# Performance work log

Hardware: AMD Instinct MI355X
Metric: run time of the kernel (lower is better)

## Reference

```python
import jax, jax.numpy as jnp
import numpy as np

DIM = 1024
HEADS = 16
DIM_HEAD = 64
INNER = HEADS * DIM_HEAD
B, M, N = 8, 4096, 256
EPS = 1e-5


def layer_norm(x, g, b):
    mu = jnp.mean(x, axis=-1, keepdims=True)
    var = jnp.mean(jnp.square(x - mu), axis=-1, keepdims=True)
    return (x - mu) * jax.lax.rsqrt(var + EPS) * g + b


def setup_inputs() -> dict:
    key = jax.random.key(0)
    ks = jax.random.split(key, 8)
    x = jax.random.normal(ks[0], (B, M, DIM), dtype=jnp.float32)
    latents = jax.random.normal(ks[1], (B, N, DIM), dtype=jnp.float32)
    x_att_mask = jax.random.randint(ks[2], (B, M), 0, 2) == 1  # True = masked
    s = 0.02
    Wq = jax.random.normal(ks[3], (DIM, INNER), dtype=jnp.float32) * s
    Wkv = jax.random.normal(ks[4], (DIM, 2 * INNER), dtype=jnp.float32) * s
    Wo = jax.random.normal(ks[5], (INNER, DIM), dtype=jnp.float32) * s
    return {
        "x": x, "latents": latents, "x_att_mask": x_att_mask,
        "nm_g": jnp.ones((DIM,), jnp.float32), "nm_b": jnp.zeros((DIM,), jnp.float32),
        "nl_g": jnp.ones((DIM,), jnp.float32), "nl_b": jnp.zeros((DIM,), jnp.float32),
        "Wq": Wq, "Wkv": Wkv, "Wo": Wo,
    }


def reference(x, latents, x_att_mask, nm_g, nm_b, nl_g, nl_b, Wq, Wkv, Wo):
    b, n, d = latents.shape
    h, dh = HEADS, DIM_HEAD
    scale = dh ** (-0.5)

    # additive mask: concat(media mask, all-False latent mask); True -> -inf, False -> +1 (faithful quirk)
    latent_mask = jnp.zeros((b, n), dtype=bool)
    full_mask = jnp.concatenate([x_att_mask, latent_mask], axis=1)  # [b, m+n]
    add_mask = jnp.where(full_mask, -jnp.inf, 1.0).astype(x.dtype)[:, None, None, :]  # [b,1,1,m+n]

    xn = layer_norm(x, nm_g, nm_b)
    ln = layer_norm(latents, nl_g, nl_b)

    q = (ln @ Wq).reshape(b, n, h, dh).transpose(0, 2, 1, 3)  # bhnd
    kv_in = jnp.concatenate([xn, ln], axis=1)                 # [b, m+n, d]
    kv = kv_in @ Wkv
    k, v = jnp.split(kv, 2, axis=-1)
    j = kv_in.shape[1]
    k = k.reshape(b, j, h, dh).transpose(0, 2, 1, 3)
    v = v.reshape(b, j, h, dh).transpose(0, 2, 1, 3)

    sim = jnp.einsum('bhid,bhjd->bhij', q * scale, k)
    sim = sim - jnp.max(sim, axis=-1, keepdims=True)
    sim = sim + add_mask
    attn = jax.nn.softmax(sim, axis=-1)
    out = jnp.einsum('bhij,bhjd->bhid', attn, v)
    out = out.transpose(0, 2, 1, 3).reshape(b, n, h * dh)
    return out @ Wo
```

## Files before the change

### kernel.cpp

```cpp
#include <hip/hip_runtime.h>
#include <hip/hip_bf16.h>
#include <stdint.h>

#define HEADS 16
#define DH    64
#define NB    8
#define MQ    256
#define MX    4096
#define JD    4352
#define DIMV  1024
#define GK    1024

typedef __bf16 bf16;
typedef __bf16 bf16x8 __attribute__((ext_vector_type(8)));
typedef float  f32x4  __attribute__((ext_vector_type(4)));

#define SWZ(r, c) (((c) ^ ((r) & 7)))

#define VMW(n) asm volatile("s_waitcnt vmcnt(" #n ")" ::: "memory")

__device__ __forceinline__ void gl_lds16(const void* g, void* l) {
  __builtin_amdgcn_global_load_lds((const __attribute__((address_space(1))) void*)g,
                                   (__attribute__((address_space(3))) void*)l, 16, 0, 0);
}

__global__ __launch_bounds__(256) void ln_kernel(
    const float* __restrict__ X, const float* __restrict__ gw, const float* __restrict__ bw,
    bf16* __restrict__ out_kv, bf16* __restrict__ out_ln, int is_lat)
{
  const int row = blockIdx.x;
  const int tid = threadIdx.x;
  const float4 v = ((const float4*)(X + (size_t)row * DIMV))[tid];
  float s  = v.x + v.y + v.z + v.w;
  float s2 = v.x*v.x + v.y*v.y + v.z*v.z + v.w*v.w;
#pragma unroll
  for (int m = 1; m < 64; m <<= 1) { s += __shfl_xor(s, m); s2 += __shfl_xor(s2, m); }
  __shared__ float red[8];
  const int wid = tid >> 6;
  if ((tid & 63) == 0) { red[wid*2] = s; red[wid*2+1] = s2; }
  __syncthreads();
  s  = red[0] + red[2] + red[4] + red[6];
  s2 = red[1] + red[3] + red[5] + red[7];
  const float mu  = s * (1.0f / DIMV);
  const float var = s2 * (1.0f / DIMV) - mu * mu;
  const float rst = rsqrtf(var + 1e-5f);
  const float4 g4 = ((const float4*)gw)[tid];
  const float4 b4 = ((const float4*)bw)[tid];
  union { bf16 h[4]; short4 s4; } u;
  u.h[0] = (bf16)((v.x - mu) * rst * g4.x + b4.x);
  u.h[1] = (bf16)((v.y - mu) * rst * g4.y + b4.y);
  u.h[2] = (bf16)((v.z - mu) * rst * g4.z + b4.z);
  u.h[3] = (bf16)((v.w - mu) * rst * g4.w + b4.w);
  size_t kvrow;
  if (is_lat) { int b = row >> 8;  int i = row & 255;  kvrow = (size_t)b * JD + MX + i; }
  else        { int b = row >> 12; int j = row & 4095; kvrow = (size_t)b * JD + j; }
  *(short4*)(out_kv + kvrow * DIMV + tid * 4) = u.s4;
  if (is_lat) *(short4*)(out_ln + (size_t)row * DIMV + tid * 4) = u.s4;
}

__global__ __launch_bounds__(256) void transpose_w(
    const float* __restrict__ in, bf16* __restrict__ out, int R, int C)
{
  __shared__ float t[64][65];
  const int tilesC = C >> 6;
  const int tc = blockIdx.x % tilesC, tr = blockIdx.x / tilesC;
  const int r0 = tr << 6, c0 = tc << 6;
  const int lr = threadIdx.x >> 4;
  const int lc = (threadIdx.x & 15) << 2;
#pragma unroll
  for (int p = 0; p < 4; p++) {
    float4 v = *(const float4*)&in[(size_t)(r0 + lr + p*16) * C + c0 + lc];
    t[lr + p*16][lc    ] = v.x; t[lr + p*16][lc + 1] = v.y;
    t[lr + p*16][lc + 2] = v.z; t[lr + p*16][lc + 3] = v.w;
  }
  __syncthreads();
#pragma unroll
  for (int p = 0; p < 4; p++) {
    const int oc = lr + p*16;
    union { bf16 h[4]; short4 s4; } u;
    u.h[0] = (bf16)t[lc    ][oc]; u.h[1] = (bf16)t[lc + 1][oc];
    u.h[2] = (bf16)t[lc + 2][oc]; u.h[3] = (bf16)t[lc + 3][oc];
    *(short4*)&out[(size_t)(c0 + oc) * R + r0 + lc] = u.s4;
  }
}

__global__ __launch_bounds__(256) void mask_detect(
    const unsigned char* __restrict__ m, int n, int* __restrict__ flag)
{
  const int tid = threadIdx.x;
  int cnt = 0;
  for (int i = tid; i < n; i += 256) cnt += (m[i] != 0) ? 1 : 0;
#pragma unroll
  for (int mm = 1; mm < 64; mm <<= 1) cnt += __shfl_xor(cnt, mm);
  __shared__ int r4[4];
  if ((tid & 63) == 0) r4[tid >> 6] = cnt;
  __syncthreads();
  if (tid == 0) {
    int t = r4[0] + r4[1] + r4[2] + r4[3];
    flag[0] = (t * 16 > n * 5) ? 1 : 0;
  }
}

__global__ __launch_bounds__(256) void mask_build(
    const void* __restrict__ mraw, const int* __restrict__ flag, float* __restrict__ mm)
{
  const int idx = blockIdx.x * 256 + threadIdx.x;
  const int b = idx / JD, j = idx - b * JD;
  float v = 1.0f;
  if (j < MX) {
    bool masked = (*flag) ? (((const unsigned char*)mraw)[b * MX + j] != 0)
                          : (((const int*)mraw)[b * MX + j] != 0);
    v = masked ? 0.0f : 1.0f;
  }
  mm[idx] = v;
}

__global__ __launch_bounds__(512, 2) void gemm256(
    const bf16* __restrict__ A, const bf16* __restrict__ Bt,
    const bf16* __restrict__ Aq, const bf16* __restrict__ Bq,
    bf16* __restrict__ outR, bf16* __restrict__ outVT, bf16* __restrict__ outQ)
{
  __shared__ bf16 sm[65536];

  const int tid = threadIdx.x;
  const int lane = tid & 63, wid = tid >> 6;
  const int wr = wid >> 2, wc = wid & 3;
  const int lc = lane & 15, lq = lane >> 4;
  const int srow = tid >> 3, sc = tid & 7;
  const int ssw = SWZ(srow, sc) * 8;

  int bid = blockIdx.x;
  bid = (bid & 7) * 140 + (bid >> 3);

  const bf16 *Arow, *Brow;
  int m0, n0, omode;
  if (bid < 1088) {
    const int by = bid >> 3, bx = bid & 7;
    m0 = by * 256;
    if (bx < 4) { n0 = bx * 256;
      Arow = A  + (size_t)m0 * GK; Brow = Bt + (size_t)n0 * GK; omode = 0; }
    else        { n0 = 1024 + (bx - 4) * 256;
      Arow = Bt + (size_t)n0 * GK; Brow = A  + (size_t)m0 * GK; omode = 1; }
  } else {
    const int ix = bid - 1088;
    m0 = (ix >> 2) * 256; n0 = (ix & 3) * 256;
    Arow = Aq + (size_t)m0 * GK; Brow = Bq + (size_t)n0 * GK; omode = 2;
  }

  const bf16* Abase = Arow + (size_t)srow * GK + ssw;
  const bf16* Bbase = Brow + (size_t)srow * GK + ssw;

  auto stA = [&](int d, int h, int kt) {
#pragma unroll
    for (int l = 0; l < 2; ++l)
      gl_lds16(Abase + (size_t)(h*128 + l*64) * GK + kt * 64,
               &sm[d*32768 + (h*128 + l*64)*64 + tid*8]);
  };
  auto stB = [&](int d, int h, int kt) {
#pragma unroll
    for (int l = 0; l < 2; ++l)
      gl_lds16(Bbase + (size_t)(h*128 + l*64) * GK + kt * 64,
               &sm[d*32768 + 16384 + (h*128 + l*64)*64 + tid*8]);
  };

  f32x4 acc[8][4];
#pragma unroll
  for (int i = 0; i < 8; i++)
#pragma unroll
    for (int j = 0; j < 4; j++)
#pragma unroll
      for (int r = 0; r < 4; r++) acc[i][j][r] = 0.f;

#define DS_PHASE(d, q, STAGE_STMT, WAIT_STMT)                                  \
  {                                                                            \
    const bf16* As_ = sm + (d)*32768;                                          \
    const bf16* Bs_ = sm + (d)*32768 + 16384;                                  \
    bf16x8 af[2][2];                                                           \
    _Pragma("unroll") for (int mi = 0; mi < 2; ++mi)                           \
      _Pragma("unroll") for (int kk = 0; kk < 2; ++kk)                         \
        af[mi][kk] = *(const bf16x8*)&As_[(wr*128 + ((q)*2+mi)*16 + lc)*64 +   \
                                          SWZ(lc, kk*4 + lq)*8];               \
    if ((q) == 0) {                                                            \
      _Pragma("unroll") for (int n = 0; n < 4; ++n)                            \
        _Pragma("unroll") for (int kk = 0; kk < 2; ++kk)                       \
          bfrag[n][kk] = *(const bf16x8*)&Bs_[(wc*64 + n*16 + lc)*64 +         \
                                              SWZ(lc, kk*4 + lq)*8];           \
    }                                                                          \
    STAGE_STMT;                                                                \
    WAIT_STMT;                                                                 \
    __builtin_amdgcn_s_barrier();                                              \
    __builtin_amdgcn_s_setprio(1);                                             \
    _Pragma("unroll") for (int kk = 0; kk < 2; ++kk)                           \
      _Pragma("unroll") for (int mi = 0; mi < 2; ++mi)                         \
        _Pragma("unroll") for (int n = 0; n < 4; ++n)                          \
          acc[(q)*2+mi][n] = __builtin_amdgcn_mfma_f32_16x16x32_bf16(          \
              af[mi][kk], bfrag[n][kk], acc[(q)*2+mi][n], 0, 0, 0);            \
    __builtin_amdgcn_s_setprio(0);                                             \
    __builtin_amdgcn_s_barrier();                                              \
  }

  stB(0, 0, 0); stB(0, 1, 0);
  stA(0, 0, 0); stA(0, 1, 0);
  stB(1, 0, 1); stB(1, 1, 1);
  VMW(4);
  __builtin_amdgcn_s_barrier();

  bf16x8 bfrag[4][2];
#pragma unroll 1
  for (int it = 0; it < 8; ++it) {
    const int tb = 2*it + 1, ta2 = 2*it + 2, tb2 = 2*it + 3;
    const bool s2 = (ta2 < 16), s3 = (tb2 < 16);
    DS_PHASE(0, 0, { stA(1, 0, tb); stA(1, 1, tb); }, {});
    DS_PHASE(0, 1, { if (s2) stB(0, 0, ta2); }, {});
    DS_PHASE(0, 2, { if (s2) stB(0, 1, ta2); }, {});
    DS_PHASE(0, 3, {}, { if (s2) { VMW(4); } else { VMW(0); } });
    DS_PHASE(1, 0, { if (s2) stA(0, 0, ta2); }, {});
    DS_PHASE(1, 1, { if (s2) stA(0, 1, ta2); }, {});
    DS_PHASE(1, 2, { if (s3) stB(1, 0, tb2); }, {});
    DS_PHASE(1, 3, { if (s3) stB(1, 1, tb2); }, { if (s3) { VMW(4); } });
  }
#undef DS_PHASE

  __syncthreads();
  bf16* Ct = sm;
#pragma unroll
  for (int m = 0; m < 8; ++m)
#pragma unroll
    for (int n = 0; n < 4; ++n) {
      const int col = wc*64 + n*16 + lc;
      const int cch = col >> 3, cw = col & 7;
#pragma unroll
      for (int r = 0; r < 4; ++r) {
        const int row = wr*128 + m*16 + lq*4 + r;
        Ct[row*256 + (((cch ^ (row & 31)) << 3) + cw)] = (bf16)acc[m][n][r];
      }
    }
  __syncthreads();

  const int cch = tid & 31, r0 = tid >> 5;
  if (omode != 1) {
    bf16* dst0 = (omode == 0 ? outR : outQ);
#pragma unroll
    for (int i = 0; i < 16; ++i) {
      const int row = r0 + i*16;
      bf16x8 v = *(const bf16x8*)&Ct[row*256 + ((cch ^ (row & 31)) << 3)];
      *(bf16x8*)(dst0 + (size_t)(m0 + row) * 1024 + n0 + cch*8) = v;
    }
  } else {
    const int bb = m0 / JD;
    const int jbase = m0 - bb * JD;
#pragma unroll
    for (int i = 0; i < 16; ++i) {
      const int row = r0 + i*16;
      const int cc = n0 + row - 1024;
      bf16x8 v = *(const bf16x8*)&Ct[row*256 + ((cch ^ (row & 31)) << 3)];
      bf16* dst = outVT + (((size_t)(bb*HEADS + (cc >> 6)))*64 + (cc & 63)) * JD
                        + jbase + cch*8;
      *(bf16x8*)dst = v;
    }
  }
}

__global__ __launch_bounds__(256) void gemm128(
    const bf16* __restrict__ A, const bf16* __restrict__ Bt,
    float* __restrict__ Cf, int N)
{
  __shared__ bf16 smem[2 * 128 * 64];
  bf16* As = smem;
  bf16* Bs = smem + 128 * 64;

  const int tid = threadIdx.x;
  const int lane = tid & 63, wid = tid >> 6;
  const int wr = wid >> 1, wc = wid & 1;
  const int m0 = blockIdx.y * 128;
  const int n0 = blockIdx.x * 128;
  const int srow = tid >> 3, sc = tid & 7;
  const int ssw = SWZ(srow, sc) * 8;
  const int lc = lane & 15, lq = lane >> 4;

  f32x4 acc[4][4];
#pragma unroll
  for (int i = 0; i < 4; i++)
#pragma unroll
    for (int j = 0; j < 4; j++)
#pragma unroll
      for (int r = 0; r < 4; r++) acc[i][j][r] = 0.f;

  const bf16* Abase = A + (size_t)m0 * GK + (size_t)srow * GK + ssw;
  const bf16* Bbase = Bt + (size_t)n0 * GK + (size_t)srow * GK + ssw;

  for (int k0 = 0; k0 < GK; k0 += 64) {
    __syncthreads();
#pragma unroll
    for (int q = 0; q < 4; q++) {
      gl_lds16(Abase + (size_t)q * 32 * GK + k0, &As[(srow + q*32) * 64 + sc*8]);
      gl_lds16(Bbase + (size_t)q * 32 * GK + k0, &Bs[(srow + q*32) * 64 + sc*8]);
    }
    VMW(0);
    __syncthreads();
#pragma unroll
    for (int kk = 0; kk < 2; kk++) {
      bf16x8 af[4], bfr[4];
#pragma unroll
      for (int mi = 0; mi < 4; mi++)
        af[mi] = *(const bf16x8*)&As[(wr*64 + mi*16 + lc) * 64 + SWZ(lc, kk*4 + lq)*8];
#pragma unroll
      for (int ni = 0; ni < 4; ni++)
        bfr[ni] = *(const bf16x8*)&Bs[(wc*64 + ni*16 + lc) * 64 + SWZ(lc, kk*4 + lq)*8];
#pragma unroll
      for (int mi = 0; mi < 4; mi++)
#pragma unroll
        for (int ni = 0; ni < 4; ni++)
          acc[mi][ni] = __builtin_amdgcn_mfma_f32_16x16x32_bf16(af[mi], bfr[ni], acc[mi][ni], 0, 0, 0);
    }
  }

#pragma unroll
  for (int mi = 0; mi < 4; mi++)
#pragma unroll
    for (int ni = 0; ni < 4; ni++) {
      const int r = m0 + wr*64 + mi*16 + lq*4;
      const int c = n0 + wc*64 + ni*16 + lc;
#pragma unroll
      for (int reg = 0; reg < 4; reg++)
        Cf[(size_t)(r + reg) * N + c] = acc[mi][ni][reg];
    }
}

__global__ __launch_bounds__(512) void attn_kernel(
    const bf16* __restrict__ Qrows,
    const bf16* __restrict__ Krows,
    const bf16* __restrict__ VT,
    const float* __restrict__ mmul,
    bf16* __restrict__ outp)
{
  const int bh = blockIdx.x >> 1, qt = blockIdx.x & 1;
  const int b = bh >> 4, h = bh & 15;
  __shared__ bf16 Qs[128 * 64];
  __shared__ bf16 Ks[2][64 * 64];
  __shared__ bf16 VTs[2][64 * 64];
  __shared__ bf16 Ps[8][16 * 64];
  const int tid = threadIdx.x, lane = tid & 63, w = tid >> 6;
  const int lc = lane & 15, lq = lane >> 4;
  const int srow = tid >> 3, sc = tid & 7;
  const int ssw = SWZ(srow, sc) * 8;

  const bf16* Qg = Qrows + ((size_t)(b*MQ + qt*128)) * 1024 + h*64;
  const bf16* Kg = Krows + ((size_t)b * JD) * 1024 + h*64;
  const bf16* Vg = VT + ((size_t)bh * 64) * JD;

  auto stKV = [&](int c, int t) {
    gl_lds16(Kg + (size_t)(t*64 + srow) * 1024 + ssw, &Ks[c][tid*8]);
    gl_lds16(Vg + (size_t)srow * JD + t*64 + ssw, &VTs[c][tid*8]);
  };

  gl_lds16(Qg + (size_t)srow * 1024 + ssw, &Qs[tid*8]);
  gl_lds16(Qg + (size_t)(srow + 64) * 1024 + ssw, &Qs[(tid + 512)*8]);
  stKV(0, 0);
  stKV(1, 1);
  VMW(2);
  __syncthreads();

  bf16x8 qf[2];
#pragma unroll
  for (int kk = 0; kk < 2; kk++)
    qf[kk] = *(const bf16x8*)&Qs[(w*16 + lc) * 64 + SWZ(lc, kk*4 + lq)*8];

  char* PsW = (char*)&Ps[w][0];
  f32x4 oacc[4];
  float den = 0.f;
#pragma unroll
  for (int di = 0; di < 4; di++)
#pragma unroll
    for (int r = 0; r < 4; r++) oacc[di][r] = 0.f;

#pragma unroll 1
  for (int t = 0; t < JD/64; ++t) {
    const int c = t & 1;
    const int j0 = t * 64;

    f32x4 sacc[4];
#pragma unroll
    for (int nj = 0; nj < 4; nj++)
#pragma unroll
      for (int r = 0; r < 4; r++) sacc[nj][r] = 0.f;
#pragma unroll
    for (int kk = 0; kk < 2; kk++) {
      bf16x8 kf[4];
#pragma unroll
      for (int nj = 0; nj < 4; nj++)
        kf[nj] = *(const bf16x8*)&Ks[c][(nj*16 + lc) * 64 + SWZ(lc, kk*4 + lq)*8];
#pragma unroll
      for (int nj = 0; nj < 4; nj++)
        sacc[nj] = __builtin_amdgcn_mfma_f32_16x16x32_bf16(kf[nj], qf[kk], sacc[nj], 0, 0, 0);
    }

#pragma unroll
    for (int nj = 0; nj < 4; nj++) {
      const float4 mm4 = *(const float4*)&mmul[b * JD + j0 + nj*16 + lq*4];
      const float p0 = exp2f(sacc[nj][0] * 0.18033688f) * mm4.x;
      const float p1 = exp2f(sacc[nj][1] * 0.18033688f) * mm4.y;
      const float p2 = exp2f(sacc[nj][2] * 0.18033688f) * mm4.z;
      const float p3 = exp2f(sacc[nj][3] * 0.18033688f) * mm4.w;
      den += (p0 + p1) + (p2 + p3);
      union { bf16 h[4]; uint2 u2; } pu;
      pu.h[0] = (bf16)p0; pu.h[1] = (bf16)p1; pu.h[2] = (bf16)p2; pu.h[3] = (bf16)p3;
      const int c4s = (nj*2 + (lq >> 1)) ^ (lc & 7);
      *(uint2*)(PsW + lc*128 + (c4s << 4) + ((lq & 1) << 3)) = pu.u2;
    }

#pragma unroll
    for (int kk = 0; kk < 2; kk++) {
      bf16x8 pf = *(const bf16x8*)(PsW + lc*128 + ((((kk << 2) + lq) ^ (lc & 7)) << 4));
#pragma unroll
      for (int di = 0; di < 4; di++) {
        bf16x8 vf = *(const bf16x8*)&VTs[c][(di*16 + lc) * 64 + SWZ(lc, kk*4 + lq)*8];
        oacc[di] = __builtin_amdgcn_mfma_f32_16x16x32_bf16(pf, vf, oacc[di], 0, 0, 0);
      }
    }

    __builtin_amdgcn_s_barrier();
    if (t + 2 < JD/64) {
      stKV(c, t + 2);
      VMW(2);
    } else if (t + 1 < JD/64) {
      VMW(0);
    }
    __builtin_amdgcn_s_barrier();
  }

  den += __shfl_xor(den, 16);
  den += __shfl_xor(den, 32);
  const float rden = 1.0f / den;

#pragma unroll
  for (int di = 0; di < 4; di++) {
    const int col = h*64 + di*16 + lc;
#pragma unroll
    for (int r = 0; r < 4; r++) {
      const float dr = __shfl(rden, lq*4 + r, 16);
      const int i = qt*128 + w*16 + lq*4 + r;
      outp[(size_t)(b*MQ + i) * 1024 + col] = (bf16)(oacc[di][r] * dr);
    }
  }
}

extern "C" void kernel_launch(void* const* d_in, const int* in_sizes, int n_in,
                              void* d_out, int out_size, void* d_ws, size_t ws_size,
                              hipStream_t stream)
{
  const float* x    = (const float*)d_in[0];
  const float* lat  = (const float*)d_in[1];
  const void*  mraw = d_in[2];
  const float* nm_g = (const float*)d_in[3];
  const float* nm_b = (const float*)d_in[4];
  const float* nl_g = (const float*)d_in[5];
  const float* nl_b = (const float*)d_in[6];
  const float* Wq   = (const float*)d_in[7];
  const float* Wkv  = (const float*)d_in[8];
  const float* Wo   = (const float*)d_in[9];
  float* out = (float*)d_out;

  char* p = (char*)d_ws;
  auto alloc = [&](size_t bytes) { char* r = p; p += (bytes + 255) & ~(size_t)255; return r; };

  bf16*  kv_in  = (bf16*)alloc((size_t)NB * JD * DIMV * 2);
  bf16*  Krows  = (bf16*)alloc((size_t)NB * JD * 1024 * 2);
  bf16*  VTbuf  = (bf16*)alloc((size_t)NB * HEADS * 64 * JD * 2);
  bf16*  WqT    = (bf16*)alloc((size_t)1024 * 1024 * 2);
  bf16*  WkvT   = (bf16*)alloc((size_t)2048 * 1024 * 2);
  bf16*  WoT    = (bf16*)alloc((size_t)1024 * 1024 * 2);
  bf16*  ln_buf = (bf16*)alloc((size_t)NB * MQ * DIMV * 2);
  bf16*  Qrows  = (bf16*)alloc((size_t)NB * MQ * 1024 * 2);
  bf16*  attout = (bf16*)alloc((size_t)NB * MQ * DIMV * 2);
  float* mmulp  = (float*)alloc((size_t)NB * JD * 4);
  int*   flag   = (int*)alloc(256);
  (void)ws_size; (void)in_sizes; (void)n_in; (void)out_size;

  ln_kernel<<<NB * MX, 256, 0, stream>>>(x,   nm_g, nm_b, kv_in, nullptr, 0);
  ln_kernel<<<NB * MQ, 256, 0, stream>>>(lat, nl_g, nl_b, kv_in, ln_buf, 1);
  transpose_w<<<256, 256, 0, stream>>>(Wq,  WqT,  1024, 1024);
  transpose_w<<<512, 256, 0, stream>>>(Wkv, WkvT, 1024, 2048);
  transpose_w<<<256, 256, 0, stream>>>(Wo,  WoT,  1024, 1024);
  mask_detect<<<1, 256, 0, stream>>>((const unsigned char*)mraw, 32768, flag);
  mask_build<<<136, 256, 0, stream>>>(mraw, flag, mmulp);

  gemm256<<<1120, 512, 0, stream>>>(kv_in, WkvT, ln_buf, WqT, Krows, VTbuf, Qrows);
  attn_kernel<<<256, 512, 0, stream>>>(Qrows, Krows, VTbuf, mmulp, attout);
  gemm128<<<dim3(8, 16), 256, 0, stream>>>(attout, WoT, out, 1024);
}
```

Measured before the change: 524.5 us.

## Deepen attention K/V prefetch to four stages and stage additive mask in LDS

The attention kernel's K/V ring buffer grows from two to four stages, so loads are issued further ahead of their use. The whole per-batch mask row is preloaded into shared memory once. The mask becomes additive (a large negative bias folded into the exp2 argument with an fma), replacing a global float4 load and a multiply every tile. This raises LDS use per block to roughly 100KB, which may cut occupancy, and the additive bias only approximates zeroing masked terms.

```diff
diff --git a/kernel.cpp b/kernel.cpp
--- a/kernel.cpp
+++ b/kernel.cpp
@@ -102,17 +102,17 @@
 }
 
 __global__ __launch_bounds__(256) void mask_build(
-    const void* __restrict__ mraw, const int* __restrict__ flag, float* __restrict__ mm)
+    const void* __restrict__ mraw, const int* __restrict__ flag, float* __restrict__ madd)
 {
   const int idx = blockIdx.x * 256 + threadIdx.x;
   const int b = idx / JD, j = idx - b * JD;
-  float v = 1.0f;
+  float v = 0.0f;
   if (j < MX) {
     bool masked = (*flag) ? (((const unsigned char*)mraw)[b * MX + j] != 0)
                           : (((const int*)mraw)[b * MX + j] != 0);
-    v = masked ? 0.0f : 1.0f;
-  }
-  mm[idx] = v;
+    v = masked ? -20000.0f : 0.0f;
+  }
+  madd[idx] = v;
 }
 
 __global__ __launch_bounds__(512, 2) void gemm256(
@@ -331,15 +331,16 @@
     const bf16* __restrict__ Qrows,
     const bf16* __restrict__ Krows,
     const bf16* __restrict__ VT,
-    const float* __restrict__ mmul,
+    const float* __restrict__ madd,
     bf16* __restrict__ outp)
 {
   const int bh = blockIdx.x >> 1, qt = blockIdx.x & 1;
   const int b = bh >> 4, h = bh & 15;
   __shared__ bf16 Qs[128 * 64];
-  __shared__ bf16 Ks[2][64 * 64];
-  __shared__ bf16 VTs[2][64 * 64];
+  __shared__ bf16 Ks[4][64 * 64];
+  __shared__ bf16 VTs[4][64 * 64];
   __shared__ bf16 Ps[8][16 * 64];
+  __shared__ float Madd[JD];
   const int tid = threadIdx.x, lane = tid & 63, w = tid >> 6;
   const int lc = lane & 15, lq = lane >> 4;
   const int srow = tid >> 3, sc = tid & 7;
@@ -348,6 +349,7 @@
   const bf16* Qg = Qrows + ((size_t)(b*MQ + qt*128)) * 1024 + h*64;
   const bf16* Kg = Krows + ((size_t)b * JD) * 1024 + h*64;
   const bf16* Vg = VT + ((size_t)bh * 64) * JD;
+  const float* mp = madd + (size_t)b * JD;
 
   auto stKV = [&](int c, int t) {
     gl_lds16(Kg + (size_t)(t*64 + srow) * 1024 + ssw, &Ks[c][tid*8]);
@@ -356,9 +358,12 @@
 
   gl_lds16(Qg + (size_t)srow * 1024 + ssw, &Qs[tid*8]);
   gl_lds16(Qg + (size_t)(srow + 64) * 1024 + ssw, &Qs[(tid + 512)*8]);
-  stKV(0, 0);
-  stKV(1, 1);
-  VMW(2);
+  gl_lds16(mp + tid*4,        &Madd[tid*4]);
+  gl_lds16(mp + 2048 + tid*4, &Madd[2048 + tid*4]);
+  if (tid < 64) gl_lds16(mp + 4096 + tid*4, &Madd[4096 + tid*4]);
+  VMW(0);
+  stKV(0, 0); stKV(1, 1); stKV(2, 2); stKV(3, 3);
+  VMW(6);
   __syncthreads();
 
   bf16x8 qf[2];
@@ -376,7 +381,7 @@
 
 #pragma unroll 1
   for (int t = 0; t < JD/64; ++t) {
-    const int c = t & 1;
+    const int c = t & 3;
     const int j0 = t * 64;
 
     f32x4 sacc[4];
@@ -397,11 +402,11 @@
 
 #pragma unroll
     for (int nj = 0; nj < 4; nj++) {
-      const float4 mm4 = *(const float4*)&mmul[b * JD + j0 + nj*16 + lq*4];
-      const float p0 = exp2f(sacc[nj][0] * 0.18033688f) * mm4.x;
-      const float p1 = exp2f(sacc[nj][1] * 0.18033688f) * mm4.y;
-      const float p2 = exp2f(sacc[nj][2] * 0.18033688f) * mm4.z;
-      const float p3 = exp2f(sacc[nj][3] * 0.18033688f) * mm4.w;
+      const float4 ma4 = *(const float4*)&Madd[j0 + nj*16 + lq*4];
+      const float p0 = exp2f(fmaf(sacc[nj][0], 0.18033688f, ma4.x));
+      const float p1 = exp2f(fmaf(sacc[nj][1], 0.18033688f, ma4.y));
+      const float p2 = exp2f(fmaf(sacc[nj][2], 0.18033688f, ma4.z));
+      const float p3 = exp2f(fmaf(sacc[nj][3], 0.18033688f, ma4.w));
       den += (p0 + p1) + (p2 + p3);
       union { bf16 h[4]; uint2 u2; } pu;
       pu.h[0] = (bf16)p0; pu.h[1] = (bf16)p1; pu.h[2] = (bf16)p2; pu.h[3] = (bf16)p3;
@@ -420,11 +425,12 @@
     }
 
     __builtin_amdgcn_s_barrier();
-    if (t + 2 < JD/64) {
-      stKV(c, t + 2);
-      VMW(2);
-    } else if (t + 1 < JD/64) {
-      VMW(0);
+    if (t + 4 < JD/64) {
+      stKV(c, t + 4);
+      VMW(6);
+    } else if (t == JD/64 - 4) { VMW(4);
+    } else if (t == JD/64 - 3) { VMW(2);
+    } else if (t == JD/64 - 2) { VMW(0);
     }
     __builtin_amdgcn_s_barrier();
   }
@@ -473,7 +479,7 @@
   bf16*  ln_buf = (bf16*)alloc((size_t)NB * MQ * DIMV * 2);
   bf16*  Qrows  = (bf16*)alloc((size_t)NB * MQ * 1024 * 2);
   bf16*  attout = (bf16*)alloc((size_t)NB * MQ * DIMV * 2);
-  float* mmulp  = (float*)alloc((size_t)NB * JD * 4);
+  float* maddp  = (float*)alloc((size_t)NB * JD * 4);
   int*   flag   = (int*)alloc(256);
   (void)ws_size; (void)in_sizes; (void)n_in; (void)out_size;
 
@@ -483,9 +489,9 @@
   transpose_w<<<512, 256, 0, stream>>>(Wkv, WkvT, 1024, 2048);
   transpose_w<<<256, 256, 0, stream>>>(Wo,  WoT,  1024, 1024);
   mask_detect<<<1, 256, 0, stream>>>((const unsigned char*)mraw, 32768, flag);
-  mask_build<<<136, 256, 0, stream>>>(mraw, flag, mmulp);
+  mask_build<<<136, 256, 0, stream>>>(mraw, flag, maddp);
 
   gemm256<<<1120, 512, 0, stream>>>(kv_in, WkvT, ln_buf, WqT, Krows, VTbuf, Qrows);
-  attn_kernel<<<256, 512, 0, stream>>>(Qrows, Krows, VTbuf, mmulp, attout);
+  attn_kernel<<<256, 512, 0, stream>>>(Qrows, Krows, VTbuf, maddp, attout);
   gemm128<<<dim3(8, 16), 256, 0, stream>>>(attout, WoT, out, 1024);
 }
```

Measured after the change: 522.8 us. Within noise of the previous version (-0.3%).
